# Kernel tuning notes

Measured on AMD Instinct MI355X. Metric: run time of the kernel, lower is better.

Reference implementation:

```python
import jax, jax.numpy as jnp
import numpy as np

N = 100000      # nodes
E = 1_000_000   # edges (avg degree ~10)
D_IN = 64
HID = 64
N_CLS = 32


def setup_inputs() -> dict:
    key = jax.random.key(0)
    ks = jax.random.split(key, 9)
    x = jax.random.normal(ks[0], (N, D_IN), dtype=jnp.float32)
    edge_index = jax.random.randint(ks[1], (2, E), 0, N, dtype=jnp.int32)
    s_in = 1.0 / np.sqrt(D_IN)
    s_h = 1.0 / np.sqrt(HID)
    W1 = jax.random.normal(ks[2], (D_IN, HID), dtype=jnp.float32) * s_in
    b1 = jnp.zeros((HID,), dtype=jnp.float32)
    W2 = jax.random.normal(ks[3], (HID, HID), dtype=jnp.float32) * s_h
    b2 = jnp.zeros((HID,), dtype=jnp.float32)
    Wl = jax.random.normal(ks[4], (HID, N_CLS), dtype=jnp.float32) * s_h
    bl = jnp.zeros((N_CLS,), dtype=jnp.float32)
    return {"x": x, "edge_index": edge_index,
            "W1": W1, "b1": b1, "W2": W2, "b2": b2, "Wl": Wl, "bl": bl}


def reference(x, edge_index, W1, b1, W2, b2, Wl, bl):
    # GCNConv default: add self-loops, symmetric normalization D^-1/2 (A+I) D^-1/2
    loop = jnp.arange(N, dtype=edge_index.dtype)
    src = jnp.concatenate([edge_index[0], loop])  # [E+N]
    dst = jnp.concatenate([edge_index[1], loop])  # [E+N]

    deg = jax.ops.segment_sum(jnp.ones_like(dst, dtype=jnp.float32), dst,
                              num_segments=N)              # [N]
    dinv = jnp.where(deg > 0, jax.lax.rsqrt(deg), 0.0)      # D^-1/2
    norm = dinv[src] * dinv[dst]                            # [E+N]

    def gcn_conv(h, W, b):
        h = h @ W                                           # [N, F_out]
        msg = h[src] * norm[:, None]                        # gather + scale
        return jax.ops.segment_sum(msg, dst, num_segments=N) + b

    h = jax.nn.relu(gcn_conv(x, W1, b1))
    h = jax.nn.relu(gcn_conv(h, W2, b2))
    return h @ Wl + bl
```

## Files before the change

### kernel.cpp

```cpp
#include <hip/hip_runtime.h>
#include <hip/hip_fp16.h>
#include <math.h>


#define TPB    256
#define TPB1   1024
#define EBLKS  256
#define BSH    7
#define BNODES (1 << BSH)

__global__ __launch_bounds__(TPB1)
void k_p1hist(const int* __restrict__ dst, int* __restrict__ OFS,
              int E, int CH, int NBC) {
    __shared__ int h[1024];
    int tid = threadIdx.x, b = blockIdx.x;
    h[tid] = 0;
    __syncthreads();
    int beg = b * CH, end = min(E, beg + CH);
    if (beg < end) {
        int nfull = (end - beg) & ~3;
        for (int i = beg + tid * 4; i < beg + nfull; i += TPB1 * 4) {
            int4 d = *(const int4*)&dst[i];
            atomicAdd(&h[d.x >> BSH], 1);
            atomicAdd(&h[d.y >> BSH], 1);
            atomicAdd(&h[d.z >> BSH], 1);
            atomicAdd(&h[d.w >> BSH], 1);
        }
        if (tid < (end - beg) - nfull)
            atomicAdd(&h[dst[beg + nfull + tid] >> BSH], 1);
    }
    __syncthreads();
    for (int c = tid; c < NBC; c += TPB1) OFS[c * EBLKS + b] = h[c];
}

__global__ __launch_bounds__(TPB)
void k_scanA(const int* __restrict__ OFS, int* __restrict__ bsum, int total) {
    __shared__ int s[TPB];
    int tid = threadIdx.x;
    int i0  = blockIdx.x * 1024 + tid * 4;
    int t = 0;
#pragma unroll
    for (int k = 0; k < 4; ++k) {
        int i = i0 + k;
        t += (i < total) ? OFS[i] : 0;
    }
    s[tid] = t;
    __syncthreads();
    for (int off = TPB / 2; off > 0; off >>= 1) {
        if (tid < off) s[tid] += s[tid + off];
        __syncthreads();
    }
    if (tid == 0) bsum[blockIdx.x] = s[0];
}

__global__ __launch_bounds__(TPB)
void k_scanC(int* __restrict__ OFS, const int* __restrict__ bsum, int total) {
    __shared__ int s[TPB];
    __shared__ int pfx;
    int tid = threadIdx.x;
    if (tid < 64) {
        int v = 0;
        for (int j = tid; j < (int)blockIdx.x; j += 64) v += bsum[j];
#pragma unroll
        for (int off = 1; off < 64; off <<= 1) v += __shfl_xor(v, off);
        if (tid == 0) pfx = v;
    }
    int i0 = blockIdx.x * 1024 + tid * 4;
    int v[4];
#pragma unroll
    for (int k = 0; k < 4; ++k) {
        int i = i0 + k;
        v[k] = (i < total) ? OFS[i] : 0;
    }
    int tsum = v[0] + v[1] + v[2] + v[3];
    s[tid] = tsum;
    __syncthreads();
    for (int off = 1; off < TPB; off <<= 1) {
        int x = (tid >= off) ? s[tid - off] : 0;
        __syncthreads();
        s[tid] += x;
        __syncthreads();
    }
    int base = pfx + (s[tid] - tsum);
#pragma unroll
    for (int k = 0; k < 4; ++k) {
        int i = i0 + k;
        if (i < total) {
            OFS[i] = base;
            base += v[k];
        }
    }
}

__global__ __launch_bounds__(TPB1)
void k_p1scatter(const int* __restrict__ src, const int* __restrict__ dst,
                 const int* __restrict__ OFS, int* __restrict__ ebuf,
                 int E, int CH, int NBC) {
    __shared__ int cur[1024];
    int tid = threadIdx.x, b = blockIdx.x;
    for (int c = tid; c < NBC; c += TPB1) cur[c] = OFS[c * EBLKS + b];
    __syncthreads();
    int beg = b * CH, end = min(E, beg + CH);
    if (beg >= end) return;
    int nfull = (end - beg) & ~3;
    for (int i = beg + tid * 4; i < beg + nfull; i += TPB1 * 4) {
        int4 s4 = *(const int4*)&src[i];
        int4 d4 = *(const int4*)&dst[i];
        int p0 = atomicAdd(&cur[d4.x >> BSH], 1);
        int p1 = atomicAdd(&cur[d4.y >> BSH], 1);
        int p2 = atomicAdd(&cur[d4.z >> BSH], 1);
        int p3 = atomicAdd(&cur[d4.w >> BSH], 1);
        ebuf[p0] = (s4.x << BSH) | (d4.x & (BNODES - 1));
        ebuf[p1] = (s4.y << BSH) | (d4.y & (BNODES - 1));
        ebuf[p2] = (s4.z << BSH) | (d4.z & (BNODES - 1));
        ebuf[p3] = (s4.w << BSH) | (d4.w & (BNODES - 1));
    }
    if (tid < (end - beg) - nfull) {
        int i = beg + nfull + tid;
        int d = dst[i];
        int p = atomicAdd(&cur[d >> BSH], 1);
        ebuf[p] = (src[i] << BSH) | (d & (BNODES - 1));
    }
}

__global__ __launch_bounds__(TPB)
void k_p2(const int* __restrict__ ebuf, const int* __restrict__ OFS,
          int* __restrict__ row_ptr, float* __restrict__ dinv,
          int* __restrict__ colw, int N, int E, int NBC) {
    __shared__ int cnt[BNODES];
    __shared__ int ofs[BNODES];
    __shared__ int s1[TPB];
    int tid = threadIdx.x, c = blockIdx.x;
    int beg = OFS[c * EBLKS];
    int end = (c == NBC - 1) ? E : OFS[(c + 1) * EBLKS];
    if (tid < BNODES) cnt[tid] = 0;
    __syncthreads();
    for (int i = beg + tid; i < end; i += TPB)
        atomicAdd(&cnt[ebuf[i] & (BNODES - 1)], 1);
    __syncthreads();
    int a = (tid < BNODES) ? cnt[tid] : 0;
    s1[tid] = a;
    __syncthreads();
    for (int off = 1; off < TPB; off <<= 1) {
        int x = (tid >= off) ? s1[tid - off] : 0;
        __syncthreads();
        s1[tid] += x;
        __syncthreads();
    }
    int ex = s1[tid] - a;
    if (tid < BNODES) {
        int node = (c << BSH) + tid;
        ofs[tid] = beg + ex;
        if (node < N) {
            row_ptr[node] = beg + ex;
            dinv[node]    = rsqrtf((float)(a + 1));
        }
        cnt[tid] = 0;
    }
    if (c == NBC - 1 && tid == 0) row_ptr[N] = E;
    __syncthreads();
    for (int i0 = beg + tid; i0 < end; i0 += TPB * 4) {
        int sv[4], dl[4], pos[4];
        int have = 0;
#pragma unroll
        for (int k = 0; k < 4; ++k) {
            int i = i0 + k * TPB;
            if (i < end) {
                int e = ebuf[i];
                sv[k] = e >> BSH;
                dl[k] = e & (BNODES - 1);
                have = k + 1;
            }
        }
#pragma unroll
        for (int k = 0; k < 4; ++k) {
            if (k < have) {
                int r  = atomicAdd(&cnt[dl[k]], 1);
                pos[k] = ofs[dl[k]] + r;
            }
        }
#pragma unroll
        for (int k = 0; k < 4; ++k)
            if (k < have) colw[pos[k]] = sv[k];
    }
}

template <int F, bool FINAL, bool HIN>
__launch_bounds__(256)
__global__ void k_mm(const void* __restrict__ in, const float* __restrict__ W,
                     const float* __restrict__ bias, const float* __restrict__ dinv,
                     void* __restrict__ out, int n) {
    __shared__ float in_s[64 * 68];
    __shared__ float w_s[64 * F];

    const int tid  = threadIdx.x;
    const int row0 = blockIdx.x * 64;

    for (int i4 = tid; i4 < (64 * F) / 4; i4 += 256)
        ((float4*)w_s)[i4] = ((const float4*)W)[i4];

    if constexpr (HIN) {
        for (int idx = tid; idx < 64 * 8; idx += 256) {
            int r  = idx >> 3;
            int c8 = idx & 7;
            uint4 u = make_uint4(0u, 0u, 0u, 0u);
            if (row0 + r < n)
                u = *(const uint4*)((const __half*)in + (size_t)(row0 + r) * 64 + c8 * 8);
            float2 f0 = __half22float2(*(__half2*)&u.x);
            float2 f1 = __half22float2(*(__half2*)&u.y);
            float2 f2 = __half22float2(*(__half2*)&u.z);
            float2 f3 = __half22float2(*(__half2*)&u.w);
            float* o = &in_s[r * 68 + c8 * 8];
            *(float4*)&o[0] = make_float4(f0.x, f0.y, f1.x, f1.y);
            *(float4*)&o[4] = make_float4(f2.x, f2.y, f3.x, f3.y);
        }
    } else {
        for (int idx = tid; idx < 64 * 16; idx += 256) {
            int r  = idx >> 4;
            int c4 = idx & 15;
            float4 v;
            if (row0 + r < n)
                v = *(const float4*)((const float*)in + (size_t)(row0 + r) * 64 + c4 * 4);
            else
                v = make_float4(0.f, 0.f, 0.f, 0.f);
            *(float4*)&in_s[r * 68 + c4 * 4] = v;
        }
    }
    __syncthreads();

    constexpr int CPT = F / 16;
    const int tx = tid & 15;
    const int ty = tid >> 4;

    float acc[4][CPT];
#pragma unroll
    for (int r = 0; r < 4; ++r)
#pragma unroll
        for (int c = 0; c < CPT; ++c) acc[r][c] = 0.f;

#pragma unroll 4
    for (int k = 0; k < 64; ++k) {
        float b[CPT];
#pragma unroll
        for (int c = 0; c < CPT; ++c) b[c] = w_s[k * F + tx * CPT + c];
#pragma unroll
        for (int r = 0; r < 4; ++r) {
            float a = in_s[(ty * 4 + r) * 68 + k];
#pragma unroll
            for (int c = 0; c < CPT; ++c) acc[r][c] = fmaf(a, b[c], acc[r][c]);
        }
    }

#pragma unroll
    for (int r = 0; r < 4; ++r) {
        int row = row0 + ty * 4 + r;
        if (row >= n) continue;
        if constexpr (FINAL) {
#pragma unroll
            for (int c = 0; c < CPT; ++c) {
                int col = tx * CPT + c;
                ((float*)out)[(size_t)row * F + col] = acc[r][c] + bias[col];
            }
        } else {
            float dd = dinv[row];
            __half2 p0 = __floats2half2_rn(acc[r][0] * dd, acc[r][1] * dd);
            __half2 p1 = __floats2half2_rn(acc[r][2] * dd, acc[r][3] * dd);
            uint2 u = make_uint2(*(unsigned*)&p0, *(unsigned*)&p1);
            *(uint2*)((__half*)out + (size_t)row * 64 + tx * 4) = u;
        }
    }
    if constexpr (!FINAL) {
        if (blockIdx.x == 0 && tid < 16)
            *(uint2*)((__half*)out + (size_t)n * 64 + tid * 4) = make_uint2(0u, 0u);
    }
}

__global__ __launch_bounds__(256)
void k_gather(const int* __restrict__ row_ptr, const int* __restrict__ colw,
              const float* __restrict__ dinv, const float* __restrict__ bias,
              const __half* __restrict__ t, __half* __restrict__ agg, int N) {
    int tid  = threadIdx.x;
    int wv   = tid >> 6;
    int lane = tid & 63;
    int g = lane >> 3;
    int p = lane & 7;
    int d = blockIdx.x * 32 + wv * 8 + g;

    int beg = 0, end = 0;
    if (d < N) { beg = row_ptr[d]; end = row_ptr[d + 1]; }

    float acc[8];
#pragma unroll
    for (int k = 0; k < 8; ++k) acc[k] = 0.f;

    for (int e = beg; e < end; e += 4) {
        int s0 = colw[e];
        int s1 = (e + 1 < end) ? colw[e + 1] : N;
        int s2 = (e + 2 < end) ? colw[e + 2] : N;
        int s3 = (e + 3 < end) ? colw[e + 3] : N;
        uint4 a0 = *(const uint4*)(t + (size_t)s0 * 64 + p * 8);
        uint4 a1 = *(const uint4*)(t + (size_t)s1 * 64 + p * 8);
        uint4 a2 = *(const uint4*)(t + (size_t)s2 * 64 + p * 8);
        uint4 a3 = *(const uint4*)(t + (size_t)s3 * 64 + p * 8);
        float2 f;
        f = __half22float2(*(__half2*)&a0.x); acc[0] += f.x; acc[1] += f.y;
        f = __half22float2(*(__half2*)&a0.y); acc[2] += f.x; acc[3] += f.y;
        f = __half22float2(*(__half2*)&a0.z); acc[4] += f.x; acc[5] += f.y;
        f = __half22float2(*(__half2*)&a0.w); acc[6] += f.x; acc[7] += f.y;
        f = __half22float2(*(__half2*)&a1.x); acc[0] += f.x; acc[1] += f.y;
        f = __half22float2(*(__half2*)&a1.y); acc[2] += f.x; acc[3] += f.y;
        f = __half22float2(*(__half2*)&a1.z); acc[4] += f.x; acc[5] += f.y;
        f = __half22float2(*(__half2*)&a1.w); acc[6] += f.x; acc[7] += f.y;
        f = __half22float2(*(__half2*)&a2.x); acc[0] += f.x; acc[1] += f.y;
        f = __half22float2(*(__half2*)&a2.y); acc[2] += f.x; acc[3] += f.y;
        f = __half22float2(*(__half2*)&a2.z); acc[4] += f.x; acc[5] += f.y;
        f = __half22float2(*(__half2*)&a2.w); acc[6] += f.x; acc[7] += f.y;
        f = __half22float2(*(__half2*)&a3.x); acc[0] += f.x; acc[1] += f.y;
        f = __half22float2(*(__half2*)&a3.y); acc[2] += f.x; acc[3] += f.y;
        f = __half22float2(*(__half2*)&a3.z); acc[4] += f.x; acc[5] += f.y;
        f = __half22float2(*(__half2*)&a3.w); acc[6] += f.x; acc[7] += f.y;
    }

    if (d < N) {
        float dd = dinv[d];
        uint4 a = *(const uint4*)(t + (size_t)d * 64 + p * 8);
        float4 b0 = *(const float4*)&bias[p * 8];
        float4 b1 = *(const float4*)&bias[p * 8 + 4];
        float2 s0 = __half22float2(*(__half2*)&a.x);
        float2 s1 = __half22float2(*(__half2*)&a.y);
        float2 s2 = __half22float2(*(__half2*)&a.z);
        float2 s3 = __half22float2(*(__half2*)&a.w);
        float o0 = fmaxf(fmaf(dd, acc[0] + s0.x, b0.x), 0.f);
        float o1 = fmaxf(fmaf(dd, acc[1] + s0.y, b0.y), 0.f);
        float o2 = fmaxf(fmaf(dd, acc[2] + s1.x, b0.z), 0.f);
        float o3 = fmaxf(fmaf(dd, acc[3] + s1.y, b0.w), 0.f);
        float o4 = fmaxf(fmaf(dd, acc[4] + s2.x, b1.x), 0.f);
        float o5 = fmaxf(fmaf(dd, acc[5] + s2.y, b1.y), 0.f);
        float o6 = fmaxf(fmaf(dd, acc[6] + s3.x, b1.z), 0.f);
        float o7 = fmaxf(fmaf(dd, acc[7] + s3.y, b1.w), 0.f);
        __half2 h0 = __floats2half2_rn(o0, o1);
        __half2 h1 = __floats2half2_rn(o2, o3);
        __half2 h2 = __floats2half2_rn(o4, o5);
        __half2 h3 = __floats2half2_rn(o6, o7);
        uint4 u = make_uint4(*(unsigned*)&h0, *(unsigned*)&h1,
                             *(unsigned*)&h2, *(unsigned*)&h3);
        *(uint4*)(agg + (size_t)d * 64 + p * 8) = u;
    }
}

extern "C" void kernel_launch(void* const* d_in, const int* in_sizes, int n_in,
                              void* d_out, int out_size, void* d_ws, size_t ws_size,
                              hipStream_t stream) {
    const float* x  = (const float*)d_in[0];
    const int*   ei = (const int*)d_in[1];
    const float* W1 = (const float*)d_in[2];
    const float* b1 = (const float*)d_in[3];
    const float* W2 = (const float*)d_in[4];
    const float* b2 = (const float*)d_in[5];
    const float* Wl = (const float*)d_in[6];
    const float* bl = (const float*)d_in[7];
    float*       out = (float*)d_out;

    const int N = in_sizes[0] / 64;
    const int E = in_sizes[1] / 2;
    const int* srcp = ei;
    const int* dstp = ei + E;

    const int NBC   = (N + BNODES - 1) / BNODES;
    const int CH    = (((E + EBLKS - 1) / EBLKS) + 3) & ~3;
    const int total = NBC * EBLKS;
    const int NBLK  = (total + 1023) / 1024;

    char*  ws  = (char*)d_ws;
    size_t off = 0;
    auto alloc = [&](size_t bytes) -> void* {
        void* p = (void*)(ws + off);
        off += (bytes + 255) & ~(size_t)255;
        return p;
    };
    int*    OFS     = (int*)alloc(((size_t)total + 1) * 4);
    int*    bsum    = (int*)alloc((size_t)NBLK * 4);
    int*    ebuf    = (int*)alloc((size_t)E * 4);
    int*    row_ptr = (int*)alloc((size_t)(N + 1) * 4);
    float*  dinv    = (float*)alloc((size_t)N * 4);
    int*    colw    = (int*)alloc((size_t)E * 4);
    __half* t1      = (__half*)alloc((size_t)(N + 1) * 64 * 2);
    __half* agg1    = (__half*)alloc((size_t)N * 64 * 2);
    __half* t2      = t1;
    __half* agg2    = agg1;

    const int nb_mm = (N + 63) / 64;
    const int nb_g  = (N + 31) / 32;

    k_p1hist   <<<EBLKS, TPB1, 0, stream>>>(dstp, OFS, E, CH, NBC);
    k_scanA    <<<NBLK,  TPB,  0, stream>>>(OFS, bsum, total);
    k_scanC    <<<NBLK,  TPB,  0, stream>>>(OFS, bsum, total);
    k_p1scatter<<<EBLKS, TPB1, 0, stream>>>(srcp, dstp, OFS, ebuf, E, CH, NBC);
    k_p2       <<<NBC,   TPB,  0, stream>>>(ebuf, OFS, row_ptr, dinv, colw, N, E, NBC);

    k_mm<64, false, false><<<nb_mm, 256, 0, stream>>>(x, W1, nullptr, dinv, t1, N);
    k_gather<<<nb_g, 256, 0, stream>>>(row_ptr, colw, dinv, b1, t1, agg1, N);

    k_mm<64, false, true><<<nb_mm, 256, 0, stream>>>(agg1, W2, nullptr, dinv, t2, N);
    k_gather<<<nb_g, 256, 0, stream>>>(row_ptr, colw, dinv, b2, t2, agg2, N);

    k_mm<32, true, true><<<nb_mm, 256, 0, stream>>>(agg2, Wl, bl, nullptr, out, N);
}
```

Before: 207.3 us.

## Fuse CSR build into one cooperative kernel and fuse final gather with head

The five CSR-construction kernels (histogram, two scan passes, scatter, per-bucket sort) become a single cooperative kernel on 256 blocks of 1024 threads, separated by grid syncs. The aim is to remove several launch gaps and small-kernel tails. The per-bucket phase now runs on 256 large blocks looping over about 782 buckets, where it used to have one 256-thread block per bucket, so parallelism in that phase drops. Separately, the second gather is fused with the final linear layer, which avoids writing and re-reading the fp16 aggregate and drops one launch.

```diff
diff --git a/kernel.cpp b/kernel.cpp
--- a/kernel.cpp
+++ b/kernel.cpp
@@ -1,6 +1,9 @@
 #include <hip/hip_runtime.h>
 #include <hip/hip_fp16.h>
+#include <hip/hip_cooperative_groups.h>
 #include <math.h>
+
+namespace cg = cooperative_groups;
 
 
 #define TPB    256
@@ -10,178 +13,169 @@
 #define BNODES (1 << BSH)
 
 __global__ __launch_bounds__(TPB1)
-void k_p1hist(const int* __restrict__ dst, int* __restrict__ OFS,
-              int E, int CH, int NBC) {
+void k_csr(const int* __restrict__ src, const int* __restrict__ dst,
+           int* __restrict__ OFS, int* __restrict__ bsum,
+           int* __restrict__ ebuf, int* __restrict__ row_ptr,
+           float* __restrict__ dinv, int* __restrict__ colw,
+           int N, int E, int CH, int NBC, int total, int CH2) {
     __shared__ int h[1024];
-    int tid = threadIdx.x, b = blockIdx.x;
+    __shared__ int s1[TPB1];
+    __shared__ int cnt[BNODES];
+    __shared__ int ofs[BNODES];
+    __shared__ int pfxs;
+    cg::grid_group grid = cg::this_grid();
+    const int tid = threadIdx.x;
+    const int b   = blockIdx.x;
+
     h[tid] = 0;
     __syncthreads();
-    int beg = b * CH, end = min(E, beg + CH);
-    if (beg < end) {
-        int nfull = (end - beg) & ~3;
-        for (int i = beg + tid * 4; i < beg + nfull; i += TPB1 * 4) {
-            int4 d = *(const int4*)&dst[i];
-            atomicAdd(&h[d.x >> BSH], 1);
-            atomicAdd(&h[d.y >> BSH], 1);
-            atomicAdd(&h[d.z >> BSH], 1);
-            atomicAdd(&h[d.w >> BSH], 1);
-        }
-        if (tid < (end - beg) - nfull)
-            atomicAdd(&h[dst[beg + nfull + tid] >> BSH], 1);
-    }
-    __syncthreads();
-    for (int c = tid; c < NBC; c += TPB1) OFS[c * EBLKS + b] = h[c];
-}
-
-__global__ __launch_bounds__(TPB)
-void k_scanA(const int* __restrict__ OFS, int* __restrict__ bsum, int total) {
-    __shared__ int s[TPB];
-    int tid = threadIdx.x;
-    int i0  = blockIdx.x * 1024 + tid * 4;
-    int t = 0;
-#pragma unroll
-    for (int k = 0; k < 4; ++k) {
-        int i = i0 + k;
-        t += (i < total) ? OFS[i] : 0;
-    }
-    s[tid] = t;
-    __syncthreads();
-    for (int off = TPB / 2; off > 0; off >>= 1) {
-        if (tid < off) s[tid] += s[tid + off];
-        __syncthreads();
-    }
-    if (tid == 0) bsum[blockIdx.x] = s[0];
-}
-
-__global__ __launch_bounds__(TPB)
-void k_scanC(int* __restrict__ OFS, const int* __restrict__ bsum, int total) {
-    __shared__ int s[TPB];
-    __shared__ int pfx;
-    int tid = threadIdx.x;
-    if (tid < 64) {
-        int v = 0;
-        for (int j = tid; j < (int)blockIdx.x; j += 64) v += bsum[j];
-#pragma unroll
-        for (int off = 1; off < 64; off <<= 1) v += __shfl_xor(v, off);
-        if (tid == 0) pfx = v;
-    }
-    int i0 = blockIdx.x * 1024 + tid * 4;
+    {
+        int beg = b * CH, end = min(E, beg + CH);
+        if (beg < end) {
+            int nfull = (end - beg) & ~3;
+            for (int i = beg + tid * 4; i < beg + nfull; i += TPB1 * 4) {
+                int4 d4 = *(const int4*)&dst[i];
+                atomicAdd(&h[d4.x >> BSH], 1);
+                atomicAdd(&h[d4.y >> BSH], 1);
+                atomicAdd(&h[d4.z >> BSH], 1);
+                atomicAdd(&h[d4.w >> BSH], 1);
+            }
+            if (tid < (end - beg) - nfull)
+                atomicAdd(&h[dst[beg + nfull + tid] >> BSH], 1);
+        }
+        __syncthreads();
+        for (int c = tid; c < NBC; c += TPB1) OFS[c * EBLKS + b] = h[c];
+    }
+    grid.sync();
+
     int v[4];
-#pragma unroll
-    for (int k = 0; k < 4; ++k) {
-        int i = i0 + k;
-        v[k] = (i < total) ? OFS[i] : 0;
-    }
-    int tsum = v[0] + v[1] + v[2] + v[3];
-    s[tid] = tsum;
-    __syncthreads();
-    for (int off = 1; off < TPB; off <<= 1) {
-        int x = (tid >= off) ? s[tid - off] : 0;
-        __syncthreads();
-        s[tid] += x;
-        __syncthreads();
-    }
-    int base = pfx + (s[tid] - tsum);
-#pragma unroll
-    for (int k = 0; k < 4; ++k) {
-        int i = i0 + k;
-        if (i < total) {
-            OFS[i] = base;
-            base += v[k];
-        }
-    }
-}
-
-__global__ __launch_bounds__(TPB1)
-void k_p1scatter(const int* __restrict__ src, const int* __restrict__ dst,
-                 const int* __restrict__ OFS, int* __restrict__ ebuf,
-                 int E, int CH, int NBC) {
-    __shared__ int cur[1024];
-    int tid = threadIdx.x, b = blockIdx.x;
-    for (int c = tid; c < NBC; c += TPB1) cur[c] = OFS[c * EBLKS + b];
-    __syncthreads();
-    int beg = b * CH, end = min(E, beg + CH);
-    if (beg >= end) return;
-    int nfull = (end - beg) & ~3;
-    for (int i = beg + tid * 4; i < beg + nfull; i += TPB1 * 4) {
-        int4 s4 = *(const int4*)&src[i];
-        int4 d4 = *(const int4*)&dst[i];
-        int p0 = atomicAdd(&cur[d4.x >> BSH], 1);
-        int p1 = atomicAdd(&cur[d4.y >> BSH], 1);
-        int p2 = atomicAdd(&cur[d4.z >> BSH], 1);
-        int p3 = atomicAdd(&cur[d4.w >> BSH], 1);
-        ebuf[p0] = (s4.x << BSH) | (d4.x & (BNODES - 1));
-        ebuf[p1] = (s4.y << BSH) | (d4.y & (BNODES - 1));
-        ebuf[p2] = (s4.z << BSH) | (d4.z & (BNODES - 1));
-        ebuf[p3] = (s4.w << BSH) | (d4.w & (BNODES - 1));
-    }
-    if (tid < (end - beg) - nfull) {
-        int i = beg + nfull + tid;
-        int d = dst[i];
-        int p = atomicAdd(&cur[d >> BSH], 1);
-        ebuf[p] = (src[i] << BSH) | (d & (BNODES - 1));
-    }
-}
-
-__global__ __launch_bounds__(TPB)
-void k_p2(const int* __restrict__ ebuf, const int* __restrict__ OFS,
-          int* __restrict__ row_ptr, float* __restrict__ dinv,
-          int* __restrict__ colw, int N, int E, int NBC) {
-    __shared__ int cnt[BNODES];
-    __shared__ int ofs[BNODES];
-    __shared__ int s1[TPB];
-    int tid = threadIdx.x, c = blockIdx.x;
-    int beg = OFS[c * EBLKS];
-    int end = (c == NBC - 1) ? E : OFS[(c + 1) * EBLKS];
-    if (tid < BNODES) cnt[tid] = 0;
-    __syncthreads();
-    for (int i = beg + tid; i < end; i += TPB)
-        atomicAdd(&cnt[ebuf[i] & (BNODES - 1)], 1);
-    __syncthreads();
-    int a = (tid < BNODES) ? cnt[tid] : 0;
-    s1[tid] = a;
-    __syncthreads();
-    for (int off = 1; off < TPB; off <<= 1) {
-        int x = (tid >= off) ? s1[tid - off] : 0;
-        __syncthreads();
-        s1[tid] += x;
-        __syncthreads();
-    }
-    int ex = s1[tid] - a;
-    if (tid < BNODES) {
-        int node = (c << BSH) + tid;
-        ofs[tid] = beg + ex;
-        if (node < N) {
-            row_ptr[node] = beg + ex;
-            dinv[node]    = rsqrtf((float)(a + 1));
-        }
-        cnt[tid] = 0;
-    }
-    if (c == NBC - 1 && tid == 0) row_ptr[N] = E;
-    __syncthreads();
-    for (int i0 = beg + tid; i0 < end; i0 += TPB * 4) {
-        int sv[4], dl[4], pos[4];
-        int have = 0;
+    int tsum = 0;
+    {
+        int i0 = b * CH2 + tid * 4;
 #pragma unroll
         for (int k = 0; k < 4; ++k) {
-            int i = i0 + k * TPB;
-            if (i < end) {
-                int e = ebuf[i];
-                sv[k] = e >> BSH;
-                dl[k] = e & (BNODES - 1);
-                have = k + 1;
-            }
-        }
+            int i = i0 + k;
+            v[k] = (tid * 4 + k < CH2 && i < total) ? OFS[i] : 0;
+            tsum += v[k];
+        }
+        s1[tid] = tsum;
+        __syncthreads();
+        for (int off = TPB1 / 2; off > 0; off >>= 1) {
+            if (tid < off) s1[tid] += s1[tid + off];
+            __syncthreads();
+        }
+        if (tid == 0) bsum[b] = s1[0];
+    }
+    grid.sync();
+
+    {
+        if (tid < 64) {
+            int vv = 0;
+            for (int j = tid; j < b; j += 64) vv += bsum[j];
+#pragma unroll
+            for (int off = 1; off < 64; off <<= 1) vv += __shfl_xor(vv, off);
+            if (tid == 0) pfxs = vv;
+        }
+        s1[tid] = tsum;
+        __syncthreads();
+        for (int off = 1; off < TPB1; off <<= 1) {
+            int x = (tid >= off) ? s1[tid - off] : 0;
+            __syncthreads();
+            s1[tid] += x;
+            __syncthreads();
+        }
+        int base = pfxs + (s1[tid] - tsum);
+        int i0 = b * CH2 + tid * 4;
 #pragma unroll
         for (int k = 0; k < 4; ++k) {
-            if (k < have) {
-                int r  = atomicAdd(&cnt[dl[k]], 1);
-                pos[k] = ofs[dl[k]] + r;
-            }
-        }
-#pragma unroll
-        for (int k = 0; k < 4; ++k)
-            if (k < have) colw[pos[k]] = sv[k];
+            int i = i0 + k;
+            if (tid * 4 + k < CH2 && i < total) { OFS[i] = base; base += v[k]; }
+        }
+    }
+    grid.sync();
+
+    {
+        for (int c = tid; c < NBC; c += TPB1) h[c] = OFS[c * EBLKS + b];
+        __syncthreads();
+        int beg = b * CH, end = min(E, beg + CH);
+        if (beg < end) {
+            int nfull = (end - beg) & ~3;
+            for (int i = beg + tid * 4; i < beg + nfull; i += TPB1 * 4) {
+                int4 s4 = *(const int4*)&src[i];
+                int4 d4 = *(const int4*)&dst[i];
+                int p0 = atomicAdd(&h[d4.x >> BSH], 1);
+                int p1 = atomicAdd(&h[d4.y >> BSH], 1);
+                int p2 = atomicAdd(&h[d4.z >> BSH], 1);
+                int p3 = atomicAdd(&h[d4.w >> BSH], 1);
+                ebuf[p0] = (s4.x << BSH) | (d4.x & (BNODES - 1));
+                ebuf[p1] = (s4.y << BSH) | (d4.y & (BNODES - 1));
+                ebuf[p2] = (s4.z << BSH) | (d4.z & (BNODES - 1));
+                ebuf[p3] = (s4.w << BSH) | (d4.w & (BNODES - 1));
+            }
+            if (tid < (end - beg) - nfull) {
+                int i = beg + nfull + tid;
+                int d = dst[i];
+                int p = atomicAdd(&h[d >> BSH], 1);
+                ebuf[p] = (src[i] << BSH) | (d & (BNODES - 1));
+            }
+        }
+    }
+    grid.sync();
+
+    for (int c = b; c < NBC; c += gridDim.x) {
+        int beg = OFS[c * EBLKS];
+        int end = (c == NBC - 1) ? E : OFS[(c + 1) * EBLKS];
+        if (tid < BNODES) cnt[tid] = 0;
+        __syncthreads();
+        for (int i = beg + tid; i < end; i += TPB1)
+            atomicAdd(&cnt[ebuf[i] & (BNODES - 1)], 1);
+        __syncthreads();
+        int a = (tid < BNODES) ? cnt[tid] : 0;
+        s1[tid] = a;
+        __syncthreads();
+        for (int off = 1; off < BNODES; off <<= 1) {
+            int x = (tid >= off && tid < BNODES) ? s1[tid - off] : 0;
+            __syncthreads();
+            if (tid < BNODES) s1[tid] += x;
+            __syncthreads();
+        }
+        int ex = s1[tid] - a;
+        if (tid < BNODES) {
+            int node = (c << BSH) + tid;
+            ofs[tid] = beg + ex;
+            if (node < N) {
+                row_ptr[node] = beg + ex;
+                dinv[node]    = rsqrtf((float)(a + 1));
+            }
+            cnt[tid] = 0;
+        }
+        if (c == NBC - 1 && tid == 0) row_ptr[N] = E;
+        __syncthreads();
+        for (int i0 = beg + tid; i0 < end; i0 += TPB1 * 4) {
+            int sv[4], dl[4], pos[4];
+            int have = 0;
+#pragma unroll
+            for (int k = 0; k < 4; ++k) {
+                int i = i0 + k * TPB1;
+                if (i < end) {
+                    int e = ebuf[i];
+                    sv[k] = e >> BSH;
+                    dl[k] = e & (BNODES - 1);
+                    have = k + 1;
+                }
+            }
+#pragma unroll
+            for (int k = 0; k < 4; ++k) {
+                if (k < have) {
+                    int r  = atomicAdd(&cnt[dl[k]], 1);
+                    pos[k] = ofs[dl[k]] + r;
+                }
+            }
+#pragma unroll
+            for (int k = 0; k < 4; ++k)
+                if (k < have) colw[pos[k]] = sv[k];
+        }
+        __syncthreads();
     }
 }
 
@@ -348,6 +342,99 @@
     }
 }
 
+__global__ __launch_bounds__(256)
+void k_gather_head(const int* __restrict__ row_ptr, const int* __restrict__ colw,
+                   const float* __restrict__ dinv, const float* __restrict__ bias,
+                   const __half* __restrict__ t, const float* __restrict__ Wl,
+                   const float* __restrict__ bl, float* __restrict__ out, int N) {
+    __shared__ float wl_s[64 * 32];
+    __shared__ float aggs[32][68];
+
+    int tid  = threadIdx.x;
+    for (int i4 = tid; i4 < (64 * 32) / 4; i4 += 256)
+        ((float4*)wl_s)[i4] = ((const float4*)Wl)[i4];
+
+    int wv   = tid >> 6;
+    int lane = tid & 63;
+    int g = lane >> 3;
+    int p = lane & 7;
+    int slot = tid >> 3;
+    int d = blockIdx.x * 32 + wv * 8 + g;
+
+    int beg = 0, end = 0;
+    if (d < N) { beg = row_ptr[d]; end = row_ptr[d + 1]; }
+
+    float acc[8];
+#pragma unroll
+    for (int k = 0; k < 8; ++k) acc[k] = 0.f;
+
+    for (int e = beg; e < end; e += 4) {
+        int s0 = colw[e];
+        int s1 = (e + 1 < end) ? colw[e + 1] : N;
+        int s2 = (e + 2 < end) ? colw[e + 2] : N;
+        int s3 = (e + 3 < end) ? colw[e + 3] : N;
+        uint4 a0 = *(const uint4*)(t + (size_t)s0 * 64 + p * 8);
+        uint4 a1 = *(const uint4*)(t + (size_t)s1 * 64 + p * 8);
+        uint4 a2 = *(const uint4*)(t + (size_t)s2 * 64 + p * 8);
+        uint4 a3 = *(const uint4*)(t + (size_t)s3 * 64 + p * 8);
+        float2 f;
+        f = __half22float2(*(__half2*)&a0.x); acc[0] += f.x; acc[1] += f.y;
+        f = __half22float2(*(__half2*)&a0.y); acc[2] += f.x; acc[3] += f.y;
+        f = __half22float2(*(__half2*)&a0.z); acc[4] += f.x; acc[5] += f.y;
+        f = __half22float2(*(__half2*)&a0.w); acc[6] += f.x; acc[7] += f.y;
+        f = __half22float2(*(__half2*)&a1.x); acc[0] += f.x; acc[1] += f.y;
+        f = __half22float2(*(__half2*)&a1.y); acc[2] += f.x; acc[3] += f.y;
+        f = __half22float2(*(__half2*)&a1.z); acc[4] += f.x; acc[5] += f.y;
+        f = __half22float2(*(__half2*)&a1.w); acc[6] += f.x; acc[7] += f.y;
+        f = __half22float2(*(__half2*)&a2.x); acc[0] += f.x; acc[1] += f.y;
+        f = __half22float2(*(__half2*)&a2.y); acc[2] += f.x; acc[3] += f.y;
+        f = __half22float2(*(__half2*)&a2.z); acc[4] += f.x; acc[5] += f.y;
+        f = __half22float2(*(__half2*)&a2.w); acc[6] += f.x; acc[7] += f.y;
+        f = __half22float2(*(__half2*)&a3.x); acc[0] += f.x; acc[1] += f.y;
+        f = __half22float2(*(__half2*)&a3.y); acc[2] += f.x; acc[3] += f.y;
+        f = __half22float2(*(__half2*)&a3.z); acc[4] += f.x; acc[5] += f.y;
+        f = __half22float2(*(__half2*)&a3.w); acc[6] += f.x; acc[7] += f.y;
+    }
+
+    if (d < N) {
+        float dd = dinv[d];
+        uint4 a = *(const uint4*)(t + (size_t)d * 64 + p * 8);
+        float4 b0 = *(const float4*)&bias[p * 8];
+        float4 b1 = *(const float4*)&bias[p * 8 + 4];
+        float2 s0 = __half22float2(*(__half2*)&a.x);
+        float2 s1 = __half22float2(*(__half2*)&a.y);
+        float2 s2 = __half22float2(*(__half2*)&a.z);
+        float2 s3 = __half22float2(*(__half2*)&a.w);
+        float o0 = fmaxf(fmaf(dd, acc[0] + s0.x, b0.x), 0.f);
+        float o1 = fmaxf(fmaf(dd, acc[1] + s0.y, b0.y), 0.f);
+        float o2 = fmaxf(fmaf(dd, acc[2] + s1.x, b0.z), 0.f);
+        float o3 = fmaxf(fmaf(dd, acc[3] + s1.y, b0.w), 0.f);
+        float o4 = fmaxf(fmaf(dd, acc[4] + s2.x, b1.x), 0.f);
+        float o5 = fmaxf(fmaf(dd, acc[5] + s2.y, b1.y), 0.f);
+        float o6 = fmaxf(fmaf(dd, acc[6] + s3.x, b1.z), 0.f);
+        float o7 = fmaxf(fmaf(dd, acc[7] + s3.y, b1.w), 0.f);
+        *(float4*)&aggs[slot][p * 8]     = make_float4(o0, o1, o2, o3);
+        *(float4*)&aggs[slot][p * 8 + 4] = make_float4(o4, o5, o6, o7);
+    }
+    __syncthreads();
+
+    if (d < N) {
+        float a0 = 0.f, a1 = 0.f, a2 = 0.f, a3 = 0.f;
+#pragma unroll 8
+        for (int k = 0; k < 64; ++k) {
+            float av = aggs[slot][k];
+            float4 w = ((const float4*)&wl_s[k * 32])[p];
+            a0 = fmaf(av, w.x, a0);
+            a1 = fmaf(av, w.y, a1);
+            a2 = fmaf(av, w.z, a2);
+            a3 = fmaf(av, w.w, a3);
+        }
+        float4 bb = *(const float4*)&bl[p * 4];
+        *(float4*)&out[(size_t)d * 32 + p * 4] =
+            make_float4(a0 + bb.x, a1 + bb.y, a2 + bb.z, a3 + bb.w);
+    }
+}
+
 extern "C" void kernel_launch(void* const* d_in, const int* in_sizes, int n_in,
                               void* d_out, int out_size, void* d_ws, size_t ws_size,
                               hipStream_t stream) {
@@ -369,7 +456,7 @@
     const int NBC   = (N + BNODES - 1) / BNODES;
     const int CH    = (((E + EBLKS - 1) / EBLKS) + 3) & ~3;
     const int total = NBC * EBLKS;
-    const int NBLK  = (total + 1023) / 1024;
+    const int CH2   = (((total + EBLKS - 1) / EBLKS) + 3) & ~3;
 
     char*  ws  = (char*)d_ws;
     size_t off = 0;
@@ -379,7 +466,7 @@
         return p;
     };
     int*    OFS     = (int*)alloc(((size_t)total + 1) * 4);
-    int*    bsum    = (int*)alloc((size_t)NBLK * 4);
+    int*    bsum    = (int*)alloc((size_t)EBLKS * 4);
     int*    ebuf    = (int*)alloc((size_t)E * 4);
     int*    row_ptr = (int*)alloc((size_t)(N + 1) * 4);
     float*  dinv    = (float*)alloc((size_t)N * 4);
@@ -387,22 +474,31 @@
     __half* t1      = (__half*)alloc((size_t)(N + 1) * 64 * 2);
     __half* agg1    = (__half*)alloc((size_t)N * 64 * 2);
     __half* t2      = t1;
-    __half* agg2    = agg1;
 
     const int nb_mm = (N + 63) / 64;
     const int nb_g  = (N + 31) / 32;
 
-    k_p1hist   <<<EBLKS, TPB1, 0, stream>>>(dstp, OFS, E, CH, NBC);
-    k_scanA    <<<NBLK,  TPB,  0, stream>>>(OFS, bsum, total);
-    k_scanC    <<<NBLK,  TPB,  0, stream>>>(OFS, bsum, total);
-    k_p1scatter<<<EBLKS, TPB1, 0, stream>>>(srcp, dstp, OFS, ebuf, E, CH, NBC);
-    k_p2       <<<NBC,   TPB,  0, stream>>>(ebuf, OFS, row_ptr, dinv, colw, N, E, NBC);
+    {
+        const int* srcv = srcp;
+        const int* dstv = dstp;
+        int* OFSv = OFS; int* bsumv = bsum; int* ebufv = ebuf;
+        int* rpv = row_ptr; float* dinvv = dinv; int* colwv = colw;
+        int Nv = N, Ev = E, CHv = CH, NBCv = NBC, totalv = total, CH2v = CH2;
+        void* kargs[] = {
+            (void*)&srcv, (void*)&dstv, (void*)&OFSv, (void*)&bsumv,
+            (void*)&ebufv, (void*)&rpv, (void*)&dinvv, (void*)&colwv,
+            (void*)&Nv, (void*)&Ev, (void*)&CHv, (void*)&NBCv,
+            (void*)&totalv, (void*)&CH2v
+        };
+        hipLaunchCooperativeKernel(k_csr, dim3(EBLKS), dim3(TPB1),
+                                   kargs, 0, stream);
+    }
 
     k_mm<64, false, false><<<nb_mm, 256, 0, stream>>>(x, W1, nullptr, dinv, t1, N);
     k_gather<<<nb_g, 256, 0, stream>>>(row_ptr, colw, dinv, b1, t1, agg1, N);
 
     k_mm<64, false, true><<<nb_mm, 256, 0, stream>>>(agg1, W2, nullptr, dinv, t2, N);
-    k_gather<<<nb_g, 256, 0, stream>>>(row_ptr, colw, dinv, b2, t2, agg2, N);
-
-    k_mm<32, true, true><<<nb_mm, 256, 0, stream>>>(agg2, Wl, bl, nullptr, out, N);
+
+    k_gather_head<<<nb_g, 256, 0, stream>>>(row_ptr, colw, dinv, b2, t2,
+                                            Wl, bl, out, N);
 }
```

After: 345.5 us. +66.6%, slower.
